# Kernel optimization log

Measured on AMD Instinct MI355X. Metric: run time of the kernel, lower is better.

## Reference

```python
import jax, jax.numpy as jnp
import numpy as np

N_NODES = 200000
N_EDGES = 6400000
IN_F, HID, OUT = 28, 16, 2


def setup_inputs() -> dict:
    key = jax.random.key(0)
    k1, k2, k3, k4 = jax.random.split(key, 4)
    x = jax.random.normal(k1, (N_NODES, IN_F), dtype=jnp.float32)
    edge_index = jax.random.randint(k2, (2, N_EDGES), 0, N_NODES, dtype=jnp.int64)
    # Glorot-ish init for the two GCNConv weights
    W1 = jax.random.normal(k3, (IN_F, HID), dtype=jnp.float32) / np.sqrt(IN_F)
    b1 = jnp.zeros((HID,), dtype=jnp.float32)
    W2 = jax.random.normal(k4, (HID, OUT), dtype=jnp.float32) / np.sqrt(HID)
    b2 = jnp.zeros((OUT,), dtype=jnp.float32)
    return {"x": x, "edge_index": edge_index, "W1": W1, "b1": b1, "W2": W2, "b2": b2}


def _gcn_conv(h, W, b, src, dst, n_nodes):
    # PyG GCNConv: h' = D^{-1/2} (A + I) D^{-1/2} (h W) + b, self-loops already in src/dst
    h = h @ W  # [N, F_out] — transform first (small F), then aggregate
    deg = jax.ops.segment_sum(jnp.ones_like(dst, dtype=h.dtype), dst, num_segments=n_nodes)
    dis = jnp.where(deg > 0, jax.lax.rsqrt(jnp.maximum(deg, 1.0)), 0.0)
    norm = dis[src] * dis[dst]                    # [E]
    msg = h[src] * norm[:, None]                  # gather + scale
    agg = jax.ops.segment_sum(msg, dst, num_segments=n_nodes)  # scatter-add
    return agg + b


def reference(x, edge_index, W1, b1, W2, b2):
    n = x.shape[0]
    loops = jnp.arange(n, dtype=edge_index.dtype)
    src = jnp.concatenate([edge_index[0], loops])  # add self-loops
    dst = jnp.concatenate([edge_index[1], loops])
    h = _gcn_conv(x, W1, b1, src, dst, n)
    h = jax.nn.relu(h)
    # F.dropout(training=self.training): inference mode -> identity
    h = _gcn_conv(h, W2, b2, src, dst, n)
    return jax.nn.log_softmax(h, axis=1)
```

## Files before the change

### kernel.cpp

```cpp
#include <hip/hip_runtime.h>
#include <hip/hip_fp16.h>
#include <math.h>

#define N_IN_F 28
#define N_HID 16
#define NPB 256
#define NBK 1024
#define EPB 8192
#define SRC_BITS 18
#define SRC_MASK ((1 << SRC_BITS) - 1)
#define STAGE_CAP 10240


__global__ void __launch_bounds__(512)
k_bhist(const int* __restrict__ dst, unsigned short* __restrict__ chunk_hist, int ne) {
    __shared__ int hist[NBK];
    int tid = threadIdx.x;
    for (int t = tid; t < NBK; t += 512) hist[t] = 0;
    __syncthreads();
    int e0 = blockIdx.x * EPB;
    int e1 = min(e0 + EPB, ne);
    for (int e = e0 + tid; e < e1; e += 512) atomicAdd(&hist[dst[e] >> 8], 1);
    __syncthreads();
    unsigned short* ch = chunk_hist + (size_t)blockIdx.x * NBK;
    for (int t = tid; t < NBK; t += 512) ch[t] = (unsigned short)hist[t];
}

__global__ void __launch_bounds__(256)
k_colscan(const unsigned short* __restrict__ chunk_hist, int* __restrict__ gdelta,
          int* __restrict__ total, int nchunk) {
    __shared__ int p[16][17];
    int tid = threadIdx.x;
    int j = tid & 15;
    int g = tid >> 4;
    int bkt = blockIdx.x * 16 + j;
    int cpg = (nchunk + 15) >> 4;
    int c0 = g * cpg, c1 = min(c0 + cpg, nchunk);

    int s = 0;
    for (int c = c0; c < c1; ++c) s += chunk_hist[(size_t)c * NBK + bkt];
    p[g][j] = s;
    __syncthreads();

    if (tid < 16) {
        int run = 0;
#pragma unroll
        for (int gg = 0; gg < 16; ++gg) { int t = p[gg][tid]; p[gg][tid] = run; run += t; }
        total[blockIdx.x * 16 + tid] = run;
    }
    __syncthreads();

    int run = p[g][j];
    for (int c = c0; c < c1; ++c) {
        int h = chunk_hist[(size_t)c * NBK + bkt];
        gdelta[(size_t)c * NBK + bkt] = run;
        run += h;
    }
}

__global__ void k_top(const int* __restrict__ total, int* __restrict__ base, int ne) {
    __shared__ int sm[NBK];
    int tid = threadIdx.x;
    int v = total[tid];
    sm[tid] = v;
    __syncthreads();
    for (int off = 1; off < NBK; off <<= 1) {
        int t = (tid >= off) ? sm[tid - off] : 0;
        __syncthreads();
        sm[tid] += t;
        __syncthreads();
    }
    base[tid] = sm[tid] - v;
    if (tid == 0) base[NBK] = ne;
}

__global__ void __launch_bounds__(1024)
k_bin(const int* __restrict__ src, const int* __restrict__ dst,
      const unsigned short* __restrict__ chunk_hist, const int* __restrict__ gdelta,
      const int* __restrict__ base, int* __restrict__ binned, int ne) {
    __shared__ int gpos[NBK];
    __shared__ int lcur[NBK];
    __shared__ int wpart[16];
    __shared__ int stage[EPB];
    __shared__ unsigned short sbid[EPB];
    int tid = threadIdx.x;
    int lane = tid & 63;
    int wid = tid >> 6;
    int chunk = blockIdx.x;

    int h = chunk_hist[(size_t)chunk * NBK + tid];
    int val = h;
#pragma unroll
    for (int off = 1; off < 64; off <<= 1) {
        int t = __shfl_up(val, off, 64);
        if (lane >= off) val += t;
    }
    if (lane == 63) wpart[wid] = val;
    __syncthreads();
    if (wid == 0) {
        int p = (lane < 16) ? wpart[lane] : 0;
#pragma unroll
        for (int off = 1; off < 16; off <<= 1) {
            int t = __shfl_up(p, off, 64);
            if (lane >= off) p += t;
        }
        if (lane < 16) wpart[lane] = p;
    }
    __syncthreads();
    int wbase = (wid > 0) ? wpart[wid - 1] : 0;
    int excl = wbase + val - h;
    gpos[tid] = base[tid] + gdelta[(size_t)chunk * NBK + tid] - excl;
    lcur[tid] = excl;
    __syncthreads();

    int e0 = chunk * EPB;
    int csz = min(EPB, ne - e0);

    for (int i = tid; i < csz; i += 1024) {
        int d = dst[e0 + i];
        int b = d >> 8;
        int r = atomicAdd(&lcur[b], 1);
        stage[r] = src[e0 + i] | ((d & (NPB - 1)) << SRC_BITS);
        sbid[r] = (unsigned short)b;
    }
    __syncthreads();

    for (int i = tid; i < csz; i += 1024) {
        binned[gpos[sbid[i]] + i] = stage[i];
    }
}

__global__ void __launch_bounds__(512)
k_sort2(const int* __restrict__ base, const int* __restrict__ binned,
        int* __restrict__ binned2, int* __restrict__ row_start,
        float* __restrict__ dis, const float* __restrict__ x,
        const float* __restrict__ W1, __half* __restrict__ hs1,
        int n, int nb_total) {
    __shared__ int cnt[NPB];
    __shared__ int pos[NPB];
    __shared__ int cur[NPB];
    __shared__ float w[N_IN_F * N_HID];
    __shared__ int stage[STAGE_CAP];
    int tid = threadIdx.x;
    if (tid < NPB) cnt[tid] = 0;
    for (int t = tid; t < N_IN_F * N_HID; t += 512) w[t] = W1[t];
    __syncthreads();

    int b = blockIdx.x;
    int e0 = base[b], e1 = base[b + 1];
    int csz = e1 - e0;

    for (int e = e0 + tid; e < e1; e += 512) atomicAdd(&cnt[binned[e] >> SRC_BITS], 1);
    __syncthreads();

    int v = (tid < NPB) ? cnt[tid] : 0;
    if (tid < NPB) pos[tid] = v;
    __syncthreads();
    for (int off = 1; off < NPB; off <<= 1) {
        int t = (tid < NPB && tid >= off) ? pos[tid - off] : 0;
        __syncthreads();
        if (tid < NPB) pos[tid] += t;
        __syncthreads();
    }
    if (tid < NPB) {
        int excl = pos[tid] - v;
        cur[tid] = excl;
        int g = b * NPB + tid;
        if (g < n) {
            row_start[g] = e0 + excl;
            dis[g] = rsqrtf((float)(v + 1));
        }
    }
    if (b == nb_total - 1 && tid == 0) row_start[n] = e1;
    __syncthreads();

    for (int e = e0 + tid; e < e1; e += 512) {
        int p = binned[e];
        int r = atomicAdd(&cur[p >> SRC_BITS], 1);
        int val = p & SRC_MASK;
        if (r < STAGE_CAP) stage[r] = val;
        else binned2[e0 + r] = val;
    }
    __syncthreads();

    int lim = min(csz, STAGE_CAP);
    for (int i = tid; i < lim; i += 512) binned2[e0 + i] = stage[i];

    if (tid < NPB) {
        int g = b * NPB + tid;
        if (g < n) {
            float di = rsqrtf((float)(cnt[tid] + 1));
            float xi[N_IN_F];
            const float4* xr = (const float4*)(x + (size_t)g * N_IN_F);
#pragma unroll
            for (int q = 0; q < N_IN_F / 4; ++q) {
                float4 vv = xr[q];
                xi[4 * q + 0] = vv.x; xi[4 * q + 1] = vv.y;
                xi[4 * q + 2] = vv.z; xi[4 * q + 3] = vv.w;
            }
            __half2 hp[N_HID / 2];
#pragma unroll
            for (int f2 = 0; f2 < N_HID / 2; ++f2) {
                float ha = 0.0f, hb = 0.0f;
#pragma unroll
                for (int k = 0; k < N_IN_F; ++k) {
                    ha = fmaf(xi[k], w[k * N_HID + 2 * f2], ha);
                    hb = fmaf(xi[k], w[k * N_HID + 2 * f2 + 1], hb);
                }
                hp[f2] = __floats2half2_rn(ha * di, hb * di);
            }
            int4* dstp = (int4*)(hs1 + (size_t)g * N_HID);
            dstp[0] = *(const int4*)&hp[0];
            dstp[1] = *(const int4*)&hp[4];
        }
    }
}


__global__ void __launch_bounds__(256)
k_agg1(const int* __restrict__ row_start, const int* __restrict__ esrc,
       const __half2* __restrict__ hs1, const float* __restrict__ dis,
       const float* __restrict__ b1, const float* __restrict__ W2,
       float2* __restrict__ hs2, int n) {
    int t = blockIdx.x * blockDim.x + threadIdx.x;
    int node = t >> 3;
    int f2 = t & 7;
    if (node >= n) return;

    int beg = row_start[node];
    int end = row_start[node + 1];
    const __half2* H = hs1 + f2;

    float2 sl = __half22float2(H[node * 8]);
    float ax = sl.x, ay = sl.y;
    float a0x = 0.f, a0y = 0.f, a1x = 0.f, a1y = 0.f;
    float a2x = 0.f, a2y = 0.f, a3x = 0.f, a3y = 0.f;
    int j = beg;
    for (; j + 16 <= end; j += 16) {
        int s[16];
#pragma unroll
        for (int q = 0; q < 16; ++q) s[q] = esrc[j + q];
        float2 v[16];
#pragma unroll
        for (int q = 0; q < 16; ++q) v[q] = __half22float2(H[s[q] * 8]);
#pragma unroll
        for (int q = 0; q < 16; q += 4) {
            a0x += v[q + 0].x; a0y += v[q + 0].y;
            a1x += v[q + 1].x; a1y += v[q + 1].y;
            a2x += v[q + 2].x; a2y += v[q + 2].y;
            a3x += v[q + 3].x; a3y += v[q + 3].y;
        }
    }
    for (; j + 4 <= end; j += 4) {
        int s0 = esrc[j], s1 = esrc[j + 1], s2 = esrc[j + 2], s3 = esrc[j + 3];
        float2 v0 = __half22float2(H[s0 * 8]);
        float2 v1 = __half22float2(H[s1 * 8]);
        float2 v2 = __half22float2(H[s2 * 8]);
        float2 v3 = __half22float2(H[s3 * 8]);
        a0x += v0.x; a0y += v0.y; a1x += v1.x; a1y += v1.y;
        a2x += v2.x; a2y += v2.y; a3x += v3.x; a3y += v3.y;
    }
    for (; j < end; ++j) {
        float2 v0 = __half22float2(H[esrc[j] * 8]);
        ax += v0.x; ay += v0.y;
    }
    ax += (a0x + a1x) + (a2x + a3x);
    ay += (a0y + a1y) + (a2y + a3y);

    float di = dis[node];
    float vx = fmaxf(fmaf(di, ax, b1[2 * f2 + 0]), 0.0f);
    float vy = fmaxf(fmaf(di, ay, b1[2 * f2 + 1]), 0.0f);
    float c0 = vx * W2[4 * f2 + 0] + vy * W2[4 * f2 + 2];
    float c1 = vx * W2[4 * f2 + 1] + vy * W2[4 * f2 + 3];
#pragma unroll
    for (int off = 4; off > 0; off >>= 1) {
        c0 += __shfl_xor(c0, off, 8);
        c1 += __shfl_xor(c1, off, 8);
    }
    if (f2 == 0) {
        float2 o;
        o.x = c0 * di;
        o.y = c1 * di;
        hs2[node] = o;
    }
}

__global__ void __launch_bounds__(256)
k_agg2(const int* __restrict__ row_start, const int* __restrict__ esrc,
       const float2* __restrict__ hs2, const float* __restrict__ dis,
       const float* __restrict__ b2, float2* __restrict__ out, int n) {
    int t = blockIdx.x * blockDim.x + threadIdx.x;
    int node = t >> 2;
    int l = t & 3;
    if (node >= n) return;

    int beg = row_start[node];
    int end = row_start[node + 1];
    float cx = 0.f, cy = 0.f;
    int j = beg + l;
    for (; j + 28 < end; j += 32) {
        int s[8];
#pragma unroll
        for (int q = 0; q < 8; ++q) s[q] = esrc[j + 4 * q];
        float2 v[8];
#pragma unroll
        for (int q = 0; q < 8; ++q) v[q] = hs2[s[q]];
#pragma unroll
        for (int q = 0; q < 8; ++q) { cx += v[q].x; cy += v[q].y; }
    }
    for (; j < end; j += 4) {
        float2 v = hs2[esrc[j]];
        cx += v.x; cy += v.y;
    }
#pragma unroll
    for (int off = 2; off > 0; off >>= 1) {
        cx += __shfl_xor(cx, off, 4);
        cy += __shfl_xor(cy, off, 4);
    }
    if (l == 0) {
        float2 self = hs2[node];
        float di = dis[node];
        float a = fmaf(di, cx + self.x, b2[0]);
        float c = fmaf(di, cy + self.y, b2[1]);
        float m = fmaxf(a, c);
        float lse = m + logf(expf(a - m) + expf(c - m));
        float2 o;
        o.x = a - lse;
        o.y = c - lse;
        out[node] = o;
    }
}


extern "C" void kernel_launch(void* const* d_in, const int* in_sizes, int n_in,
                              void* d_out, int out_size, void* d_ws, size_t ws_size,
                              hipStream_t stream) {
    const float* x  = (const float*)d_in[0];
    const int*   ei = (const int*)d_in[1];
    const float* W1 = (const float*)d_in[2];
    const float* b1 = (const float*)d_in[3];
    const float* W2 = (const float*)d_in[4];
    const float* b2 = (const float*)d_in[5];
    float2* out = (float2*)d_out;

    const int n  = in_sizes[0] / N_IN_F;
    const int ne = in_sizes[1] / 2;
    const int* src = ei;
    const int* dst = ei + ne;
    const int nb = (n + NPB - 1) / NPB;
    const int nchunk = (ne + EPB - 1) / EPB;

    int* ws_i = (int*)d_ws;
    int* total     = ws_i;
    int* base      = total + 1024;
    int* row_start = base + 1028;
    float* dis     = (float*)(row_start + n + 4);
    float2* hs2    = (float2*)(dis + n);
    __half* hs1    = (__half*)(hs2 + n);
    unsigned short* chunk_hist = (unsigned short*)((int*)hs1 + 8 * (size_t)n);
    int* binned2   = (int*)chunk_hist + ((size_t)nchunk * NBK + 1) / 2;
    int* binned    = binned2 + ne;
    int* gdelta    = binned2;

    const int B = 256;

    k_bhist<<<dim3(nchunk), dim3(512), 0, stream>>>(dst, chunk_hist, ne);
    k_colscan<<<dim3(NBK / 16), dim3(B), 0, stream>>>(chunk_hist, gdelta, total, nchunk);
    k_top<<<dim3(1), dim3(NBK), 0, stream>>>(total, base, ne);
    k_bin<<<dim3(nchunk), dim3(1024), 0, stream>>>(src, dst, chunk_hist, gdelta, base, binned, ne);
    k_sort2<<<dim3(nb), dim3(512), 0, stream>>>(base, binned, binned2, row_start, dis,
                                                x, W1, hs1, n, nb);
    {
        long long tot = (long long)n * 8;
        k_agg1<<<dim3((unsigned)((tot + B - 1) / B)), dim3(B), 0, stream>>>(
            row_start, binned2, (const __half2*)hs1, dis, b1, W2, hs2, n);
    }
    {
        long long tot = (long long)n * 4;
        k_agg2<<<dim3((unsigned)((tot + B - 1) / B)), dim3(B), 0, stream>>>(
            row_start, binned2, hs2, dis, b2, out, n);
    }
}
```

Measured before the change: 180.3 us.

## Widen histogram and sort blocks to 1024 threads, wave-shuffle scan, split feature transform

Launches the bucket-histogram and per-bucket sort kernels with 1024 threads instead of 512. The sort kernel's barrier-heavy shared-memory Hillis-Steele scan is replaced by a wavefront shuffle scan plus a small per-wave partial-sum combine. The first-layer feature transform is split across four threads per node, each computing four output features. This adds parallelism and cuts barriers, but each thread re-reads the node's full input row, and larger blocks may lower occupancy per CU.

Result: faster. 173.7 us (-3.7%).

```diff
diff --git a/kernel.cpp b/kernel.cpp
--- a/kernel.cpp
+++ b/kernel.cpp
@@ -12,18 +12,18 @@
 #define STAGE_CAP 10240
 
 
-__global__ void __launch_bounds__(512)
+__global__ void __launch_bounds__(1024)
 k_bhist(const int* __restrict__ dst, unsigned short* __restrict__ chunk_hist, int ne) {
     __shared__ int hist[NBK];
     int tid = threadIdx.x;
-    for (int t = tid; t < NBK; t += 512) hist[t] = 0;
+    if (tid < NBK) hist[tid] = 0;
     __syncthreads();
     int e0 = blockIdx.x * EPB;
     int e1 = min(e0 + EPB, ne);
-    for (int e = e0 + tid; e < e1; e += 512) atomicAdd(&hist[dst[e] >> 8], 1);
+    for (int e = e0 + tid; e < e1; e += 1024) atomicAdd(&hist[dst[e] >> 8], 1);
     __syncthreads();
     unsigned short* ch = chunk_hist + (size_t)blockIdx.x * NBK;
-    for (int t = tid; t < NBK; t += 512) ch[t] = (unsigned short)hist[t];
+    if (tid < NBK) ch[tid] = (unsigned short)hist[tid];
 }
 
 __global__ void __launch_bounds__(256)
@@ -130,51 +130,59 @@
     }
 }
 
-__global__ void __launch_bounds__(512)
+__global__ void __launch_bounds__(1024)
 k_sort2(const int* __restrict__ base, const int* __restrict__ binned,
         int* __restrict__ binned2, int* __restrict__ row_start,
         float* __restrict__ dis, const float* __restrict__ x,
         const float* __restrict__ W1, __half* __restrict__ hs1,
         int n, int nb_total) {
     __shared__ int cnt[NPB];
-    __shared__ int pos[NPB];
     __shared__ int cur[NPB];
+    __shared__ int wpart[4];
     __shared__ float w[N_IN_F * N_HID];
     __shared__ int stage[STAGE_CAP];
     int tid = threadIdx.x;
+    int lane = tid & 63;
+    int wv = tid >> 6;
     if (tid < NPB) cnt[tid] = 0;
-    for (int t = tid; t < N_IN_F * N_HID; t += 512) w[t] = W1[t];
+    if (tid < N_IN_F * N_HID) w[tid] = W1[tid];
     __syncthreads();
 
     int b = blockIdx.x;
     int e0 = base[b], e1 = base[b + 1];
     int csz = e1 - e0;
 
-    for (int e = e0 + tid; e < e1; e += 512) atomicAdd(&cnt[binned[e] >> SRC_BITS], 1);
-    __syncthreads();
-
-    int v = (tid < NPB) ? cnt[tid] : 0;
-    if (tid < NPB) pos[tid] = v;
-    __syncthreads();
-    for (int off = 1; off < NPB; off <<= 1) {
-        int t = (tid < NPB && tid >= off) ? pos[tid - off] : 0;
-        __syncthreads();
-        if (tid < NPB) pos[tid] += t;
-        __syncthreads();
-    }
+    for (int e = e0 + tid; e < e1; e += 1024) atomicAdd(&cnt[binned[e] >> SRC_BITS], 1);
+    __syncthreads();
+
+    int deg = 0, incl = 0;
     if (tid < NPB) {
-        int excl = pos[tid] - v;
+        deg = cnt[tid];
+        incl = deg;
+#pragma unroll
+        for (int off = 1; off < 64; off <<= 1) {
+            int t = __shfl_up(incl, off, 64);
+            if (lane >= off) incl += t;
+        }
+        if (lane == 63) wpart[wv] = incl;
+    }
+    __syncthreads();
+    if (tid < NPB) {
+        int wbase = 0;
+#pragma unroll
+        for (int q = 0; q < 4; ++q) wbase += (q < wv) ? wpart[q] : 0;
+        int excl = wbase + incl - deg;
         cur[tid] = excl;
         int g = b * NPB + tid;
         if (g < n) {
             row_start[g] = e0 + excl;
-            dis[g] = rsqrtf((float)(v + 1));
+            dis[g] = rsqrtf((float)(deg + 1));
         }
     }
     if (b == nb_total - 1 && tid == 0) row_start[n] = e1;
     __syncthreads();
 
-    for (int e = e0 + tid; e < e1; e += 512) {
+    for (int e = e0 + tid; e < e1; e += 1024) {
         int p = binned[e];
         int r = atomicAdd(&cur[p >> SRC_BITS], 1);
         int val = p & SRC_MASK;
@@ -184,12 +192,14 @@
     __syncthreads();
 
     int lim = min(csz, STAGE_CAP);
-    for (int i = tid; i < lim; i += 512) binned2[e0 + i] = stage[i];
-
-    if (tid < NPB) {
-        int g = b * NPB + tid;
+    for (int i = tid; i < lim; i += 1024) binned2[e0 + i] = stage[i];
+
+    {
+        int ln = tid >> 2;
+        int fq = tid & 3;
+        int g = b * NPB + ln;
         if (g < n) {
-            float di = rsqrtf((float)(cnt[tid] + 1));
+            float di = rsqrtf((float)(cnt[ln] + 1));
             float xi[N_IN_F];
             const float4* xr = (const float4*)(x + (size_t)g * N_IN_F);
 #pragma unroll
@@ -198,20 +208,22 @@
                 xi[4 * q + 0] = vv.x; xi[4 * q + 1] = vv.y;
                 xi[4 * q + 2] = vv.z; xi[4 * q + 3] = vv.w;
             }
-            __half2 hp[N_HID / 2];
-#pragma unroll
-            for (int f2 = 0; f2 < N_HID / 2; ++f2) {
+            __half2 hp[2];
+#pragma unroll
+            for (int h2i = 0; h2i < 2; ++h2i) {
+                int f = 4 * fq + 2 * h2i;
                 float ha = 0.0f, hb = 0.0f;
 #pragma unroll
                 for (int k = 0; k < N_IN_F; ++k) {
-                    ha = fmaf(xi[k], w[k * N_HID + 2 * f2], ha);
-                    hb = fmaf(xi[k], w[k * N_HID + 2 * f2 + 1], hb);
+                    ha = fmaf(xi[k], w[k * N_HID + f], ha);
+                    hb = fmaf(xi[k], w[k * N_HID + f + 1], hb);
                 }
-                hp[f2] = __floats2half2_rn(ha * di, hb * di);
+                hp[h2i] = __floats2half2_rn(ha * di, hb * di);
             }
-            int4* dstp = (int4*)(hs1 + (size_t)g * N_HID);
-            dstp[0] = *(const int4*)&hp[0];
-            dstp[1] = *(const int4*)&hp[4];
+            int2 o;
+            o.x = *(const int*)&hp[0];
+            o.y = *(const int*)&hp[1];
+            ((int2*)(hs1 + (size_t)g * N_HID))[fq] = o;
         }
     }
 }
@@ -364,12 +376,12 @@
 
     const int B = 256;
 
-    k_bhist<<<dim3(nchunk), dim3(512), 0, stream>>>(dst, chunk_hist, ne);
+    k_bhist<<<dim3(nchunk), dim3(1024), 0, stream>>>(dst, chunk_hist, ne);
     k_colscan<<<dim3(NBK / 16), dim3(B), 0, stream>>>(chunk_hist, gdelta, total, nchunk);
     k_top<<<dim3(1), dim3(NBK), 0, stream>>>(total, base, ne);
     k_bin<<<dim3(nchunk), dim3(1024), 0, stream>>>(src, dst, chunk_hist, gdelta, base, binned, ne);
-    k_sort2<<<dim3(nb), dim3(512), 0, stream>>>(base, binned, binned2, row_start, dis,
-                                                x, W1, hs1, n, nb);
+    k_sort2<<<dim3(nb), dim3(1024), 0, stream>>>(base, binned, binned2, row_start, dis,
+                                                 x, W1, hs1, n, nb);
     {
         long long tot = (long long)n * 8;
         k_agg1<<<dim3((unsigned)((tot + B - 1) / B)), dim3(B), 0, stream>>>(
```
